# Performance work log

Measured on AMD Instinct MI355X. Metric: run time of the kernel, lower is better.

Reference implementation:

```python
import jax, jax.numpy as jnp
import numpy as np

MRG = 0.1
ALPHA = 32.0
STAT_WEIGHT = 0.01
STAT_ADJUST_WEIGHT = 0.15
COS_EPS = 1e-8  # torch F.cosine_similarity eps


def l2_norm(x):
    # matches torch l2_norm: x / sqrt(sum(x^2, axis=1) + 1e-12)
    normp = jnp.sum(x * x, axis=1) + 1e-12
    return x / jnp.sqrt(normp)[:, None]


def setup_inputs() -> dict:
    key = jax.random.key(0)
    kx, kt, kp, kc = jax.random.split(key, 4)
    B, C, D = 512, 50000, 128
    X = jax.random.normal(kx, (B, D), dtype=jnp.float32)
    T = jax.random.randint(kt, (B,), 0, C, dtype=jnp.int32)
    proxies = jax.random.normal(kp, (C, D), dtype=jnp.float32)
    class_centers = jax.random.normal(kc, (C, D), dtype=jnp.float32)
    return {"X": X, "T": T, "proxies": proxies, "class_centers": class_centers}


def reference(X, T, proxies, class_centers):
    C = proxies.shape[0]
    Xn = l2_norm(X)                      # (B, D)
    Pn = l2_norm(proxies)                # (C, D)
    cos = Xn @ Pn.T                      # (B, C)

    # ---- vectorized per-class statistics (replaces the Python loop) ----
    counts = jax.ops.segment_sum(jnp.ones(T.shape[0], jnp.float32), T, num_segments=C)
    sums = jax.ops.segment_sum(Xn, T, num_segments=C)          # (C, D)
    sqs = jax.ops.segment_sum(Xn * Xn, T, num_segments=C)      # (C, D)
    safe = jnp.maximum(counts, 1.0)[:, None]
    mean = sums / safe
    var = jnp.clip(sqs / safe - mean * mean, 1e-6, 10.0)        # biased var, clamped
    var_weight = 1.0 / (1.0 + var.mean(axis=1))                 # (C,)

    # cosine_similarity(P_norm[i], class_centers[i]) with torch eps semantics
    pnorm = jnp.maximum(jnp.sqrt(jnp.sum(Pn * Pn, axis=1)), COS_EPS)
    cnorm = jnp.maximum(jnp.sqrt(jnp.sum(class_centers * class_centers, axis=1)), COS_EPS)
    center_sim = jnp.sum(Pn * class_centers, axis=1) / (pnorm * cnorm)  # (C,)

    has_samples = counts > 0
    adj = jnp.where(has_samples, center_sim * var_weight * STAT_ADJUST_WEIGHT, 0.0)
    combined = cos + adj[None, :]        # (B, C)

    # ---- proxy-anchor exp-sum terms ----
    onehot = (T[:, None] == jnp.arange(C, dtype=T.dtype)[None, :])  # (B, C) bool
    pos_exp = jnp.exp(-ALPHA * (combined - MRG))
    neg_exp = jnp.exp(ALPHA * (combined + MRG))
    P_sim_sum = jnp.sum(jnp.where(onehot, pos_exp, 0.0), axis=0)    # (C,)
    N_sim_sum = jnp.sum(jnp.where(onehot, 0.0, neg_exp), axis=0)    # (C,)

    num_valid = jnp.sum(has_samples).astype(jnp.float32)
    pos_term = jnp.sum(jnp.log1p(P_sim_sum)) / num_valid
    neg_term = jnp.sum(jnp.log1p(N_sim_sum)) / jnp.float32(C)

    center_reg = jnp.mean(jnp.abs(class_centers))
    return pos_term + neg_term + STAT_WEIGHT * center_reg
```

## Files before the change

kernel.cpp:

```cpp
#include <hip/hip_runtime.h>
#include <math.h>

#define ALPHA 32.0f
#define MRG 0.1f
#define STAT_WEIGHT 0.01f
#define STAT_ADJ_W 0.15f
#define COS_EPS 1e-8f

typedef __attribute__((ext_vector_type(8))) short bf16x8;
typedef __attribute__((ext_vector_type(4))) float f32x4;
typedef __attribute__((ext_vector_type(4))) unsigned int u32x4;

__device__ __forceinline__ ushort f2bf(float f) {
    unsigned u = __float_as_uint(f);
    return (ushort)((u + 0x7FFFu + ((u >> 16) & 1u)) >> 16);
}
__device__ __forceinline__ unsigned pk2(float a, float b) {
    return (unsigned)f2bf(a) | ((unsigned)f2bf(b) << 16);
}

__device__ __forceinline__ float bred128(float v, float* sm, int d) {
    #pragma unroll
    for (int off = 1; off < 64; off <<= 1) v += __shfl_xor(v, off);
    if ((d & 63) == 0) sm[d >> 6] = v;
    __syncthreads();
    float r = sm[0] + sm[1];
    __syncthreads();
    return r;
}

__global__ void k_stats(const float* __restrict__ X, const float* __restrict__ proxies,
                        const float* __restrict__ cc, const int* __restrict__ T,
                        ushort* __restrict__ Xn16, float* __restrict__ adj,
                        float* __restrict__ scal, int B) {
    const int b = blockIdx.x, d = threadIdx.x;
    __shared__ int Tl[512];
    __shared__ float sm[2];
    __shared__ int mlist[512];
    __shared__ int mcnt;
    for (int i = d; i < B; i += 128) Tl[i] = T[i];
    if (d == 0) mcnt = 0;
    __syncthreads();
    const int c = Tl[b];

    float x = X[(size_t)b * 128 + d];
    float n2 = bred128(x * x, sm, d);
    float xn = x * rsqrtf(n2 + 1e-12f);
    const int pk = ((((d >> 3) ^ (b & 15)) << 3) | (d & 7));
    Xn16[(size_t)b * 128 + pk] = f2bf(xn);

    for (int j = d; j < B; j += 128)
        if (Tl[j] == c) mlist[atomicAdd(&mcnt, 1)] = j;
    __syncthreads();
    const int cnt = mcnt;
    int minj = mlist[0];
    for (int i = 1; i < cnt; ++i) minj = min(minj, mlist[i]);
    if (minj != b) return;

    float sd = 0.f, qd = 0.f;
    int prev = -1;
    for (int rank = 0; rank < cnt; ++rank) {
        int cur = 0x7fffffff;
        for (int i = 0; i < cnt; ++i) { int v = mlist[i]; if (v > prev && v < cur) cur = v; }
        prev = cur;
        float xj = X[(size_t)cur * 128 + d];
        float nj = bred128(xj * xj, sm, d);
        float xnj = xj * rsqrtf(nj + 1e-12f);
        sd += xnj; qd += xnj * xnj;
    }
    float fc = (float)cnt;
    float m = sd / fc;
    float var = fminf(fmaxf(qd / fc - m * m, 1e-6f), 10.0f);
    float sv = bred128(var, sm, d);

    float p  = proxies[(size_t)c * 128 + d];
    float cv = cc[(size_t)c * 128 + d];
    float s2 = bred128(p * p, sm, d);
    float c2 = bred128(cv * cv, sm, d);
    float pc = bred128(p * cv, sm, d);
    if (d == 0) {
        float inv = rsqrtf(s2 + 1e-12f);
        float pn = fmaxf(sqrtf(s2) * inv, COS_EPS);
        float cn = fmaxf(sqrtf(c2), COS_EPS);
        float censim = (pc * inv) / (pn * cn);
        float vw = 1.0f / (1.0f + sv * (1.0f / 128.0f));
        adj[c] = censim * vw * STAT_ADJ_W;
        atomicAdd(&scal[3], 1.0f);
    }
}

__launch_bounds__(256, 2)
__global__ void k_main(const float* __restrict__ proxies, const float* __restrict__ cc,
                       const ushort* __restrict__ Xsw, const int* __restrict__ T,
                       float* __restrict__ Psum, float* __restrict__ Nsum,
                       float* __restrict__ scal, int C) {
    const int tid = threadIdx.x, lane = tid & 63, wv = tid >> 6;
    const int nlo = lane & 15, quad = lane >> 4;
    const int c0 = blockIdx.x * 128;
    const int half = blockIdx.y;
    const int r0 = half * 256;

    __shared__ ushort Sx[16384];
    __shared__ alignas(16) int Tl[256];
    __shared__ float red[4];
    Tl[tid] = T[r0 + tid];

    float cabs = 0.f;
    if (half == 0) {
        const int n4 = ((c0 + 128 <= C) ? 128 : (C - c0)) * 32;
        const float4* cp = (const float4*)(cc + (size_t)c0 * 128);
        #pragma unroll 4
        for (int i = tid; i < n4; i += 256) {
            float4 v = cp[i];
            cabs += fabsf(v.x) + fabsf(v.y) + fabsf(v.z) + fabsf(v.w);
        }
    }

    const int cls0 = c0 + wv * 32 + nlo;
    const int cls1 = cls0 + 16;
    bf16x8 bfr[2][4];
    #pragma unroll
    for (int t = 0; t < 2; ++t) {
        int cls = c0 + wv * 32 + t * 16 + nlo;
        int cl = (cls < C) ? cls : C - 1;
        const float4* pr = (const float4*)(proxies + (size_t)cl * 128);
        float4 v0[4], v1[4];
        float s2 = 0.f;
        #pragma unroll
        for (int ks = 0; ks < 4; ++ks) {
            v0[ks] = pr[ks * 8 + quad * 2];
            v1[ks] = pr[ks * 8 + quad * 2 + 1];
            s2 += v0[ks].x*v0[ks].x + v0[ks].y*v0[ks].y + v0[ks].z*v0[ks].z + v0[ks].w*v0[ks].w
                + v1[ks].x*v1[ks].x + v1[ks].y*v1[ks].y + v1[ks].z*v1[ks].z + v1[ks].w*v1[ks].w;
        }
        s2 += __shfl_xor(s2, 16);
        s2 += __shfl_xor(s2, 32);
        float pin = rsqrtf(s2 + 1e-12f);
        #pragma unroll
        for (int ks = 0; ks < 4; ++ks) {
            u32x4 u;
            u.x = pk2(v0[ks].x * pin, v0[ks].y * pin);
            u.y = pk2(v0[ks].z * pin, v0[ks].w * pin);
            u.z = pk2(v1[ks].x * pin, v1[ks].y * pin);
            u.w = pk2(v1[ks].z * pin, v1[ks].w * pin);
            bfr[t][ks] = __builtin_bit_cast(bf16x8, u);
        }
    }

    int fro[4];
    #pragma unroll
    for (int ks = 0; ks < 4; ++ks)
        fro[ks] = nlo * 128 + (((ks * 4 + quad) ^ nlo) << 3);

    const uint4* gX = (const uint4*)Xsw + half * 4096;
    uint4 s0, s1, s2v, s3;
    #define LOADV(ch) { const uint4* p_ = gX + (ch) * 1024 + tid; \
                        s0 = p_[0]; s1 = p_[256]; s2v = p_[512]; s3 = p_[768]; }
    #define WRITEV(bi) { uint4* q_ = (uint4*)&Sx[(bi) * 8192]; \
                         q_[tid] = s0; q_[tid + 256] = s1; q_[tid + 512] = s2v; q_[tid + 768] = s3; }
    LOADV(0); WRITEV(0); LOADV(1);
    __syncthreads();

    float pp0 = 0.f, np0 = 0.f, pp1 = 0.f, np1 = 0.f;
    for (int chunk = 0; chunk < 4; ++chunk) {
        const int bo = (chunk & 1) * 8192;
        if (chunk < 3) {
            WRITEV((chunk + 1) & 1);
            if (chunk < 2) LOADV(chunk + 2);
        }
        #pragma unroll
        for (int rt = 0; rt < 4; ++rt) {
            const ushort* sb = &Sx[bo + rt * 2048];
            bf16x8 a0 = *(const bf16x8*)&sb[fro[0]];
            bf16x8 a1 = *(const bf16x8*)&sb[fro[1]];
            bf16x8 a2 = *(const bf16x8*)&sb[fro[2]];
            bf16x8 a3 = *(const bf16x8*)&sb[fro[3]];
            f32x4 acc0 = {0.f,0.f,0.f,0.f}, acc1 = {0.f,0.f,0.f,0.f};
            acc0 = __builtin_amdgcn_mfma_f32_16x16x32_bf16(a0, bfr[0][0], acc0, 0, 0, 0);
            acc1 = __builtin_amdgcn_mfma_f32_16x16x32_bf16(a0, bfr[1][0], acc1, 0, 0, 0);
            acc0 = __builtin_amdgcn_mfma_f32_16x16x32_bf16(a1, bfr[0][1], acc0, 0, 0, 0);
            acc1 = __builtin_amdgcn_mfma_f32_16x16x32_bf16(a1, bfr[1][1], acc1, 0, 0, 0);
            acc0 = __builtin_amdgcn_mfma_f32_16x16x32_bf16(a2, bfr[0][2], acc0, 0, 0, 0);
            acc1 = __builtin_amdgcn_mfma_f32_16x16x32_bf16(a2, bfr[1][2], acc1, 0, 0, 0);
            acc0 = __builtin_amdgcn_mfma_f32_16x16x32_bf16(a3, bfr[0][3], acc0, 0, 0, 0);
            acc1 = __builtin_amdgcn_mfma_f32_16x16x32_bf16(a3, bfr[1][3], acc1, 0, 0, 0);

            int4 t4 = *(const int4*)&Tl[chunk * 64 + rt * 16 + quad * 4];
            int tvs[4] = {t4.x, t4.y, t4.z, t4.w};
            #pragma unroll
            for (int r = 0; r < 4; ++r) {
                { bool po = (tvs[r] == cls0); float v = acc0[r];
                  float e = __expf(po ? -ALPHA * (v - MRG) : ALPHA * (v + MRG));
                  pp0 += po ? e : 0.f; np0 += po ? 0.f : e; }
                { bool po = (tvs[r] == cls1); float v = acc1[r];
                  float e = __expf(po ? -ALPHA * (v - MRG) : ALPHA * (v + MRG));
                  pp1 += po ? e : 0.f; np1 += po ? 0.f : e; }
            }
        }
        __syncthreads();
    }
    #undef LOADV
    #undef WRITEV

    pp0 += __shfl_xor(pp0, 16); pp0 += __shfl_xor(pp0, 32);
    np0 += __shfl_xor(np0, 16); np0 += __shfl_xor(np0, 32);
    pp1 += __shfl_xor(pp1, 16); pp1 += __shfl_xor(pp1, 32);
    np1 += __shfl_xor(np1, 16); np1 += __shfl_xor(np1, 32);
    if (quad == 0) {
        if (cls0 < C) { atomicAdd(&Psum[cls0], pp0); atomicAdd(&Nsum[cls0], np0); }
        if (cls1 < C) { atomicAdd(&Psum[cls1], pp1); atomicAdd(&Nsum[cls1], np1); }
    }

    if (half == 0) {
        #pragma unroll
        for (int off = 1; off < 64; off <<= 1) cabs += __shfl_xor(cabs, off);
        if (lane == 0) red[wv] = cabs;
        __syncthreads();
        if (tid == 0) atomicAdd(&scal[2], red[0] + red[1] + red[2] + red[3]);
    }
}

__launch_bounds__(256)
__global__ void k_fin(const float* __restrict__ Psum, const float* __restrict__ Nsum,
                      const float* __restrict__ adj, float* __restrict__ scal,
                      float* __restrict__ out, int C, int nfin) {
    const int tid = threadIdx.x, lane = tid & 63, wv = tid >> 6;
    const int c = blockIdx.x * 256 + tid;
    __shared__ float red[4][2];
    float lp = 0.f, ln = 0.f;
    if (c < C) {
        float p = Psum[c], n = Nsum[c];
        float a = (p > 0.f) ? adj[c] : 0.f;
        lp = log1pf(p * __expf(-ALPHA * a));
        ln = log1pf(n * __expf( ALPHA * a));
    }
    #pragma unroll
    for (int off = 1; off < 64; off <<= 1) {
        lp += __shfl_xor(lp, off);
        ln += __shfl_xor(ln, off);
    }
    if (lane == 0) { red[wv][0] = lp; red[wv][1] = ln; }
    __syncthreads();
    if (tid == 0) {
        atomicAdd(&scal[0], red[0][0] + red[1][0] + red[2][0] + red[3][0]);
        atomicAdd(&scal[1], red[0][1] + red[1][1] + red[2][1] + red[3][1]);
        __threadfence();
        unsigned old = atomicAdd((unsigned*)(scal + 4), 1u);
        if (old == (unsigned)(nfin - 1)) {
            float S0 = atomicAdd(&scal[0], 0.f);
            float S1 = atomicAdd(&scal[1], 0.f);
            float S2 = atomicAdd(&scal[2], 0.f);
            float S3 = atomicAdd(&scal[3], 0.f);
            out[0] = S0 / S3 + S1 / (float)C + STAT_WEIGHT * (S2 / ((float)C * 128.f));
        }
    }
}

extern "C" void kernel_launch(void* const* d_in, const int* in_sizes, int n_in,
                              void* d_out, int out_size, void* d_ws, size_t ws_size,
                              hipStream_t stream) {
    const float* X       = (const float*)d_in[0];
    const int*   T       = (const int*)d_in[1];
    const float* proxies = (const float*)d_in[2];
    const float* cc      = (const float*)d_in[3];
    float* out = (float*)d_out;

    const int B = in_sizes[1];
    const int D = in_sizes[0] / B;
    const int C = in_sizes[2] / D;

    float*  Psum = (float*)d_ws;
    float*  Nsum = Psum + C;
    float*  scal = Nsum + C;
    float*  adj  = scal + 8;
    ushort* Xn16 = (ushort*)(adj + C);

    const int nblk = (C + 127) / 128;
    const int nfin = (C + 255) / 256;

    (void)hipMemsetAsync(Psum, 0, (2 * (size_t)C + 8) * sizeof(float), stream);
    k_stats<<<B, 128, 0, stream>>>(X, proxies, cc, T, Xn16, adj, scal, B);
    k_main<<<dim3(nblk, 2), 256, 0, stream>>>(proxies, cc, Xn16, T, Psum, Nsum, scal, C);
    k_fin<<<nfin, 256, 0, stream>>>(Psum, Nsum, adj, scal, out, C, nfin);
}
```

Baseline: 135.7 us.

## Fold memset and finalize kernel into stats and main kernels

The workspace memset is replaced by a grid-stride zeroing loop at the start of k_stats. The separate k_fin kernel is removed: each k_main column block bumps a per-column done counter, and whichever of the two row-half blocks finishes second computes the log1p terms for its 128 classes. That block also counts classes with samples and feeds the global last-block reduction that writes the output. This removes one memset and one kernel launch, plus the gaps between them, at the cost of extra atomics and a device-scope fence at the end of every k_main block.

```diff
diff --git a/kernel.cpp b/kernel.cpp
--- a/kernel.cpp
+++ b/kernel.cpp
@@ -32,12 +32,15 @@
 __global__ void k_stats(const float* __restrict__ X, const float* __restrict__ proxies,
                         const float* __restrict__ cc, const int* __restrict__ T,
                         ushort* __restrict__ Xn16, float* __restrict__ adj,
-                        float* __restrict__ scal, int B) {
+                        float* __restrict__ zbase, int nzero, int B) {
     const int b = blockIdx.x, d = threadIdx.x;
     __shared__ int Tl[512];
     __shared__ float sm[2];
     __shared__ int mlist[512];
     __shared__ int mcnt;
+
+    for (int i = b * 128 + d; i < nzero; i += B * 128) zbase[i] = 0.f;
+
     for (int i = d; i < B; i += 128) Tl[i] = T[i];
     if (d == 0) mcnt = 0;
     __syncthreads();
@@ -85,7 +88,6 @@
         float censim = (pc * inv) / (pn * cn);
         float vw = 1.0f / (1.0f + sv * (1.0f / 128.0f));
         adj[c] = censim * vw * STAT_ADJ_W;
-        atomicAdd(&scal[3], 1.0f);
     }
 }
 
@@ -93,7 +95,9 @@
 __global__ void k_main(const float* __restrict__ proxies, const float* __restrict__ cc,
                        const ushort* __restrict__ Xsw, const int* __restrict__ T,
                        float* __restrict__ Psum, float* __restrict__ Nsum,
-                       float* __restrict__ scal, int C) {
+                       const float* __restrict__ adj, unsigned* __restrict__ done,
+                       float* __restrict__ scal, float* __restrict__ out,
+                       int C, int nblk) {
     const int tid = threadIdx.x, lane = tid & 63, wv = tid >> 6;
     const int nlo = lane & 15, quad = lane >> 4;
     const int c0 = blockIdx.x * 128;
@@ -103,6 +107,8 @@
     __shared__ ushort Sx[16384];
     __shared__ alignas(16) int Tl[256];
     __shared__ float red[4];
+    __shared__ float red3[4][3];
+    __shared__ unsigned dflag;
     Tl[tid] = T[r0 + tid];
 
     float cabs = 0.f;
@@ -218,19 +224,20 @@
         __syncthreads();
         if (tid == 0) atomicAdd(&scal[2], red[0] + red[1] + red[2] + red[3]);
     }
-}
-
-__launch_bounds__(256)
-__global__ void k_fin(const float* __restrict__ Psum, const float* __restrict__ Nsum,
-                      const float* __restrict__ adj, float* __restrict__ scal,
-                      float* __restrict__ out, int C, int nfin) {
-    const int tid = threadIdx.x, lane = tid & 63, wv = tid >> 6;
-    const int c = blockIdx.x * 256 + tid;
-    __shared__ float red[4][2];
-    float lp = 0.f, ln = 0.f;
-    if (c < C) {
-        float p = Psum[c], n = Nsum[c];
-        float a = (p > 0.f) ? adj[c] : 0.f;
+
+    __syncthreads();
+    __threadfence();
+    if (tid == 0) dflag = atomicAdd(&done[blockIdx.x], 1u);
+    __syncthreads();
+    if (dflag != 1u) return;
+
+    const int c = c0 + tid;
+    float lp = 0.f, ln = 0.f, nv = 0.f;
+    if (tid < 128 && c < C) {
+        float p = atomicAdd(&Psum[c], 0.f);
+        float n = atomicAdd(&Nsum[c], 0.f);
+        float a = 0.f;
+        if (p > 0.f) { a = adj[c]; nv = 1.f; }
         lp = log1pf(p * __expf(-ALPHA * a));
         ln = log1pf(n * __expf( ALPHA * a));
     }
@@ -238,15 +245,17 @@
     for (int off = 1; off < 64; off <<= 1) {
         lp += __shfl_xor(lp, off);
         ln += __shfl_xor(ln, off);
-    }
-    if (lane == 0) { red[wv][0] = lp; red[wv][1] = ln; }
+        nv += __shfl_xor(nv, off);
+    }
+    if (lane == 0) { red3[wv][0] = lp; red3[wv][1] = ln; red3[wv][2] = nv; }
     __syncthreads();
     if (tid == 0) {
-        atomicAdd(&scal[0], red[0][0] + red[1][0] + red[2][0] + red[3][0]);
-        atomicAdd(&scal[1], red[0][1] + red[1][1] + red[2][1] + red[3][1]);
+        atomicAdd(&scal[0], red3[0][0] + red3[1][0] + red3[2][0] + red3[3][0]);
+        atomicAdd(&scal[1], red3[0][1] + red3[1][1] + red3[2][1] + red3[3][1]);
+        atomicAdd(&scal[3], red3[0][2] + red3[1][2] + red3[2][2] + red3[3][2]);
         __threadfence();
         unsigned old = atomicAdd((unsigned*)(scal + 4), 1u);
-        if (old == (unsigned)(nfin - 1)) {
+        if (old == (unsigned)(nblk - 1)) {
             float S0 = atomicAdd(&scal[0], 0.f);
             float S1 = atomicAdd(&scal[1], 0.f);
             float S2 = atomicAdd(&scal[2], 0.f);
@@ -269,17 +278,17 @@
     const int D = in_sizes[0] / B;
     const int C = in_sizes[2] / D;
 
-    float*  Psum = (float*)d_ws;
-    float*  Nsum = Psum + C;
-    float*  scal = Nsum + C;
-    float*  adj  = scal + 8;
-    ushort* Xn16 = (ushort*)(adj + C);
-
-    const int nblk = (C + 127) / 128;
-    const int nfin = (C + 255) / 256;
-
-    (void)hipMemsetAsync(Psum, 0, (2 * (size_t)C + 8) * sizeof(float), stream);
-    k_stats<<<B, 128, 0, stream>>>(X, proxies, cc, T, Xn16, adj, scal, B);
-    k_main<<<dim3(nblk, 2), 256, 0, stream>>>(proxies, cc, Xn16, T, Psum, Nsum, scal, C);
-    k_fin<<<nfin, 256, 0, stream>>>(Psum, Nsum, adj, scal, out, C, nfin);
-}
+    float*    Psum = (float*)d_ws;
+    float*    Nsum = Psum + C;
+    float*    scal = Nsum + C;
+    unsigned* done = (unsigned*)(scal + 8);
+    float*    adj  = (float*)(done + 512);
+    ushort*   Xn16 = (ushort*)(adj + C);
+
+    const int nblk  = (C + 127) / 128;
+    const int nzero = 2 * C + 8 + 512;
+
+    k_stats<<<B, 128, 0, stream>>>(X, proxies, cc, T, Xn16, adj, Psum, nzero, B);
+    k_main<<<dim3(nblk, 2), 256, 0, stream>>>(proxies, cc, Xn16, T, Psum, Nsum,
+                                              adj, done, scal, out, C, nblk);
+}
```

Measured after the change: 169.5 us. 25.0% more time.

## Split batch into quarters, move memset and center abs-sum into stats kernel

Applied to the files above, without the earlier changes.

The main kernel grid now splits the batch into four 128-row slices instead of two, doubling the number of blocks. Each pair of slices accumulates into its own P/N buffer, which lowers atomic contention, and the final kernel sums the two buffers. The workspace memset is replaced by zeroing inside k_stats. The class-center abs-sum and the valid-class count are moved out of k_main and k_stats into k_stats partials and k_fin. The cost is that proxies get loaded and normalized twice as often across blocks, and k_stats does more serial work.

```diff
diff --git a/kernel.cpp b/kernel.cpp
--- a/kernel.cpp
+++ b/kernel.cpp
@@ -32,15 +32,35 @@
 __global__ void k_stats(const float* __restrict__ X, const float* __restrict__ proxies,
                         const float* __restrict__ cc, const int* __restrict__ T,
                         ushort* __restrict__ Xn16, float* __restrict__ adj,
-                        float* __restrict__ scal, int B) {
+                        float* __restrict__ zbase, int nzero,
+                        float* __restrict__ cabs_part, int C, int B) {
     const int b = blockIdx.x, d = threadIdx.x;
     __shared__ int Tl[512];
     __shared__ float sm[2];
+    __shared__ float smc[2];
     __shared__ int mlist[512];
     __shared__ int mcnt;
+
+    for (int i = b * 128 + d; i < nzero; i += B * 128) zbase[i] = 0.f;
+
     for (int i = d; i < B; i += 128) Tl[i] = T[i];
     if (d == 0) mcnt = 0;
-    __syncthreads();
+
+    float cabs = 0.f;
+    {
+        const float4* cp = (const float4*)cc;
+        const int n4 = C * 32;
+        for (int i = b * 128 + d; i < n4; i += B * 128) {
+            float4 v = cp[i];
+            cabs += fabsf(v.x) + fabsf(v.y) + fabsf(v.z) + fabsf(v.w);
+        }
+    }
+    #pragma unroll
+    for (int off = 1; off < 64; off <<= 1) cabs += __shfl_xor(cabs, off);
+    if ((d & 63) == 0) smc[d >> 6] = cabs;
+    __syncthreads();
+    if (d == 0) cabs_part[b] = smc[0] + smc[1];
+
     const int c = Tl[b];
 
     float x = X[(size_t)b * 128 + d];
@@ -85,36 +105,25 @@
         float censim = (pc * inv) / (pn * cn);
         float vw = 1.0f / (1.0f + sv * (1.0f / 128.0f));
         adj[c] = censim * vw * STAT_ADJ_W;
-        atomicAdd(&scal[3], 1.0f);
     }
 }
 
 __launch_bounds__(256, 2)
-__global__ void k_main(const float* __restrict__ proxies, const float* __restrict__ cc,
-                       const ushort* __restrict__ Xsw, const int* __restrict__ T,
-                       float* __restrict__ Psum, float* __restrict__ Nsum,
-                       float* __restrict__ scal, int C) {
+__global__ void k_main(const float* __restrict__ proxies, const ushort* __restrict__ Xsw,
+                       const int* __restrict__ T, float* __restrict__ PN,
+                       int C) {
     const int tid = threadIdx.x, lane = tid & 63, wv = tid >> 6;
     const int nlo = lane & 15, quad = lane >> 4;
     const int c0 = blockIdx.x * 128;
-    const int half = blockIdx.y;
-    const int r0 = half * 256;
+    const int q = blockIdx.y;
+    const int r0 = q * 128;
 
     __shared__ ushort Sx[16384];
-    __shared__ alignas(16) int Tl[256];
-    __shared__ float red[4];
-    Tl[tid] = T[r0 + tid];
-
-    float cabs = 0.f;
-    if (half == 0) {
-        const int n4 = ((c0 + 128 <= C) ? 128 : (C - c0)) * 32;
-        const float4* cp = (const float4*)(cc + (size_t)c0 * 128);
-        #pragma unroll 4
-        for (int i = tid; i < n4; i += 256) {
-            float4 v = cp[i];
-            cabs += fabsf(v.x) + fabsf(v.y) + fabsf(v.z) + fabsf(v.w);
-        }
-    }
+    __shared__ alignas(16) int Tl[128];
+    if (tid < 128) Tl[tid] = T[r0 + tid];
+
+    float* P = PN + (size_t)(q >> 1) * 2 * C;
+    float* N = P + C;
 
     const int cls0 = c0 + wv * 32 + nlo;
     const int cls1 = cls0 + 16;
@@ -152,7 +161,7 @@
     for (int ks = 0; ks < 4; ++ks)
         fro[ks] = nlo * 128 + (((ks * 4 + quad) ^ nlo) << 3);
 
-    const uint4* gX = (const uint4*)Xsw + half * 4096;
+    const uint4* gX = (const uint4*)Xsw + q * 2048;
     uint4 s0, s1, s2v, s3;
     #define LOADV(ch) { const uint4* p_ = gX + (ch) * 1024 + tid; \
                         s0 = p_[0]; s1 = p_[256]; s2v = p_[512]; s3 = p_[768]; }
@@ -162,12 +171,9 @@
     __syncthreads();
 
     float pp0 = 0.f, np0 = 0.f, pp1 = 0.f, np1 = 0.f;
-    for (int chunk = 0; chunk < 4; ++chunk) {
-        const int bo = (chunk & 1) * 8192;
-        if (chunk < 3) {
-            WRITEV((chunk + 1) & 1);
-            if (chunk < 2) LOADV(chunk + 2);
-        }
+    for (int chunk = 0; chunk < 2; ++chunk) {
+        const int bo = chunk * 8192;
+        if (chunk < 1) WRITEV(1);
         #pragma unroll
         for (int rt = 0; rt < 4; ++rt) {
             const ushort* sb = &Sx[bo + rt * 2048];
@@ -207,30 +213,24 @@
     pp1 += __shfl_xor(pp1, 16); pp1 += __shfl_xor(pp1, 32);
     np1 += __shfl_xor(np1, 16); np1 += __shfl_xor(np1, 32);
     if (quad == 0) {
-        if (cls0 < C) { atomicAdd(&Psum[cls0], pp0); atomicAdd(&Nsum[cls0], np0); }
-        if (cls1 < C) { atomicAdd(&Psum[cls1], pp1); atomicAdd(&Nsum[cls1], np1); }
-    }
-
-    if (half == 0) {
-        #pragma unroll
-        for (int off = 1; off < 64; off <<= 1) cabs += __shfl_xor(cabs, off);
-        if (lane == 0) red[wv] = cabs;
-        __syncthreads();
-        if (tid == 0) atomicAdd(&scal[2], red[0] + red[1] + red[2] + red[3]);
+        if (cls0 < C) { atomicAdd(&P[cls0], pp0); atomicAdd(&N[cls0], np0); }
+        if (cls1 < C) { atomicAdd(&P[cls1], pp1); atomicAdd(&N[cls1], np1); }
     }
 }
 
 __launch_bounds__(256)
-__global__ void k_fin(const float* __restrict__ Psum, const float* __restrict__ Nsum,
-                      const float* __restrict__ adj, float* __restrict__ scal,
+__global__ void k_fin(const float* __restrict__ PN, const float* __restrict__ adj,
+                      const float* __restrict__ cabs_part, float* __restrict__ scal,
                       float* __restrict__ out, int C, int nfin) {
     const int tid = threadIdx.x, lane = tid & 63, wv = tid >> 6;
     const int c = blockIdx.x * 256 + tid;
-    __shared__ float red[4][2];
-    float lp = 0.f, ln = 0.f;
+    __shared__ float red[4][3];
+    float lp = 0.f, ln = 0.f, nv = 0.f;
     if (c < C) {
-        float p = Psum[c], n = Nsum[c];
-        float a = (p > 0.f) ? adj[c] : 0.f;
+        float p = PN[c] + PN[2 * (size_t)C + c];
+        float n = PN[(size_t)C + c] + PN[3 * (size_t)C + c];
+        float a = 0.f;
+        if (p > 0.f) { a = adj[c]; nv = 1.f; }
         lp = log1pf(p * __expf(-ALPHA * a));
         ln = log1pf(n * __expf( ALPHA * a));
     }
@@ -238,12 +238,25 @@
     for (int off = 1; off < 64; off <<= 1) {
         lp += __shfl_xor(lp, off);
         ln += __shfl_xor(ln, off);
-    }
-    if (lane == 0) { red[wv][0] = lp; red[wv][1] = ln; }
+        nv += __shfl_xor(nv, off);
+    }
+    if (lane == 0) { red[wv][0] = lp; red[wv][1] = ln; red[wv][2] = nv; }
     __syncthreads();
     if (tid == 0) {
         atomicAdd(&scal[0], red[0][0] + red[1][0] + red[2][0] + red[3][0]);
         atomicAdd(&scal[1], red[0][1] + red[1][1] + red[2][1] + red[3][1]);
+        atomicAdd(&scal[3], red[0][2] + red[1][2] + red[2][2] + red[3][2]);
+    }
+    if (blockIdx.x == 0) {
+        float cb = cabs_part[tid] + cabs_part[tid + 256];
+        #pragma unroll
+        for (int off = 1; off < 64; off <<= 1) cb += __shfl_xor(cb, off);
+        __syncthreads();
+        if (lane == 0) red[wv][0] = cb;
+        __syncthreads();
+        if (tid == 0) atomicAdd(&scal[2], red[0][0] + red[1][0] + red[2][0] + red[3][0]);
+    }
+    if (tid == 0) {
         __threadfence();
         unsigned old = atomicAdd((unsigned*)(scal + 4), 1u);
         if (old == (unsigned)(nfin - 1)) {
@@ -269,17 +282,18 @@
     const int D = in_sizes[0] / B;
     const int C = in_sizes[2] / D;
 
-    float*  Psum = (float*)d_ws;
-    float*  Nsum = Psum + C;
-    float*  scal = Nsum + C;
-    float*  adj  = scal + 8;
+    float*  PN   = (float*)d_ws;
+    float*  scal = PN + 4 * (size_t)C;
+    float*  cabs_part = scal + 8;
+    float*  adj  = cabs_part + 512;
     ushort* Xn16 = (ushort*)(adj + C);
 
-    const int nblk = (C + 127) / 128;
-    const int nfin = (C + 255) / 256;
-
-    (void)hipMemsetAsync(Psum, 0, (2 * (size_t)C + 8) * sizeof(float), stream);
-    k_stats<<<B, 128, 0, stream>>>(X, proxies, cc, T, Xn16, adj, scal, B);
-    k_main<<<dim3(nblk, 2), 256, 0, stream>>>(proxies, cc, Xn16, T, Psum, Nsum, scal, C);
-    k_fin<<<nfin, 256, 0, stream>>>(Psum, Nsum, adj, scal, out, C, nfin);
-}
+    const int nblk  = (C + 127) / 128;
+    const int nfin  = (C + 255) / 256;
+    const int nzero = 4 * C + 8;
+
+    k_stats<<<B, 128, 0, stream>>>(X, proxies, cc, T, Xn16, adj, PN, nzero,
+                                   cabs_part, C, B);
+    k_main<<<dim3(nblk, 4), 256, 0, stream>>>(proxies, Xn16, T, PN, C);
+    k_fin<<<nfin, 256, 0, stream>>>(PN, adj, cabs_part, scal, out, C, nfin);
+}
```

Measured after the change: 131.8 us. 2.8% less time.
